# Optimization experiments

Hardware: AMD Instinct MI355X
Metric: run time of the kernel (lower is better)

The kernel has to match this reference:

```python
import math
import jax, jax.numpy as jnp
import numpy as np

SCALES = (128.0, 256.0, 512.0)
ASPECT_RATIOS = (0.5, 1.0, 2.0)
NMS_THR = 0.7
PRENMS_K = 6000   # rpn_test_prenms_topk (module built with training=False)
POST_K = 300      # rpn_test_topk
MIN_SIZE = 16.0
DW_CLIP = math.log(1000.0 / 16.0)


def conv2d(x, w, b, pad):
    y = jax.lax.conv_general_dilated(
        x, w, window_strides=(1, 1), padding=[(pad, pad), (pad, pad)],
        dimension_numbers=("NCHW", "OIHW", "NCHW"))
    return y + b[None, :, None, None]


def generate_anchors(im_h, im_w, grid_h, grid_w, dtype):
    stride_h = float(im_h // grid_h)
    stride_w = float(im_w // grid_w)
    ar = jnp.asarray(ASPECT_RATIOS, dtype)
    sc = jnp.asarray(SCALES, dtype)
    h_ratios = jnp.sqrt(ar)
    w_ratios = 1.0 / h_ratios
    hs = (h_ratios[:, None] * sc[None, :]).reshape(-1)   # [A]
    ws = (w_ratios[:, None] * sc[None, :]).reshape(-1)
    base = jnp.round(jnp.stack([-ws, -hs, ws, hs], axis=1) / 2.0)  # [A,4]
    xs = jnp.arange(grid_w, dtype=dtype) * stride_w
    ys = jnp.arange(grid_h, dtype=dtype) * stride_h
    sy, sx = jnp.meshgrid(ys, xs, indexing="ij")
    sx = sx.reshape(-1); sy = sy.reshape(-1)
    shift = jnp.stack([sx, sy, sx, sy], axis=1)           # [HW,4]
    return (shift[:, None, :] + base[None, :, :]).reshape(-1, 4)  # [HW*A,4]


def decode_boxes(pred, anchors):
    # pred, anchors: [N,4] -> decoded [N,4]
    w = anchors[:, 2] - anchors[:, 0]
    h = anchors[:, 3] - anchors[:, 1]
    cx = anchors[:, 0] + 0.5 * w
    cy = anchors[:, 1] + 0.5 * h
    dx, dy = pred[:, 0], pred[:, 1]
    dw = jnp.minimum(pred[:, 2], DW_CLIP)
    dh = jnp.minimum(pred[:, 3], DW_CLIP)
    px = dx * w + cx
    py = dy * h + cy
    pw = jnp.exp(dw) * w
    ph = jnp.exp(dh) * h
    return jnp.stack([px - 0.5 * pw, py - 0.5 * ph, px + 0.5 * pw, py + 0.5 * ph], axis=1)


def nms_keep(boxes, valid, thr):
    # boxes assumed sorted by descending score; sequential greedy NMS.
    N = boxes.shape[0]
    area = (boxes[:, 2] - boxes[:, 0]) * (boxes[:, 3] - boxes[:, 1])
    idx = jnp.arange(N)

    def body(i, keep):
        b = jax.lax.dynamic_slice(boxes, (i, 0), (1, 4))[0]
        x1 = jnp.maximum(b[0], boxes[:, 0])
        y1 = jnp.maximum(b[1], boxes[:, 1])
        x2 = jnp.minimum(b[2], boxes[:, 2])
        y2 = jnp.minimum(b[3], boxes[:, 3])
        inter = jnp.clip(x2 - x1, 0.0) * jnp.clip(y2 - y1, 0.0)
        iou = inter / (area[i] + area - inter)
        suppress = (iou > thr) & (idx > i) & keep[i]
        return keep & ~suppress

    return jax.lax.fori_loop(0, N, body, valid)


def rpn_forward(image, feat, rpn_conv_w, rpn_conv_b, cls_w, cls_b, bbox_w, bbox_b):
    rpn_feat = jax.nn.relu(conv2d(feat, rpn_conv_w, rpn_conv_b, pad=1))
    cls_scores = conv2d(rpn_feat, cls_w, cls_b, pad=0)       # [B,A,H,W]
    box_pred = conv2d(rpn_feat, bbox_w, bbox_b, pad=0)       # [B,4A,H,W]
    B, A, H, W = cls_scores.shape
    im_h, im_w = image.shape[-2], image.shape[-1]
    anchors = generate_anchors(im_h, im_w, H, W, feat.dtype)  # [HWA,4]

    cls_flat = jnp.transpose(cls_scores, (0, 2, 3, 1)).reshape(-1)              # [B*H*W*A]
    pred = jnp.transpose(box_pred.reshape(B, A, 4, H, W), (0, 3, 4, 1, 2)).reshape(-1, 4)
    proposals = decode_boxes(pred, anchors)                   # [N,4]

    scores = jax.nn.sigmoid(cls_flat)
    top_scores, top_idx = jax.lax.top_k(scores, PRENMS_K)
    props = proposals[top_idx]                                # [K,4]
    # clamp to image boundary
    props = jnp.stack([
        jnp.clip(props[:, 0], 0.0, float(im_w)),
        jnp.clip(props[:, 1], 0.0, float(im_h)),
        jnp.clip(props[:, 2], 0.0, float(im_w)),
        jnp.clip(props[:, 3], 0.0, float(im_h))], axis=1)
    w = props[:, 2] - props[:, 0]
    h = props[:, 3] - props[:, 1]
    valid = (w >= MIN_SIZE) & (h >= MIN_SIZE)
    keep = nms_keep(props, valid, NMS_THR)                    # already score-sorted
    masked = jnp.where(keep, top_scores, -jnp.inf)
    final_scores, sel = jax.lax.top_k(masked, POST_K)
    final_boxes = props[sel]
    ok = jnp.isfinite(final_scores)
    final_boxes = jnp.where(ok[:, None], final_boxes, 0.0)
    final_scores = jnp.where(ok, final_scores, 0.0)
    return jnp.concatenate([final_boxes, final_scores[:, None]], axis=1)  # [POST_K,5]


def setup_inputs() -> dict:
    key = jax.random.key(0)
    ks = jax.random.split(key, 6)
    C, H, W, A = 256, 128, 128, 9
    IMH = IMW = 1024
    std = 0.01
    return {
        "image": jax.random.normal(ks[0], (1, 3, IMH, IMW), jnp.float32),
        "feat": jax.random.normal(ks[1], (1, C, H, W), jnp.float32),
        "rpn_conv_w": jax.random.normal(ks[2], (C, C, 3, 3), jnp.float32) * std,
        "rpn_conv_b": jnp.zeros((C,), jnp.float32),
        "cls_w": jax.random.normal(ks[3], (A, C, 1, 1), jnp.float32) * std,
        "cls_b": jnp.zeros((A,), jnp.float32),
        "bbox_w": jax.random.normal(ks[4], (4 * A, C, 1, 1), jnp.float32) * std,
        "bbox_b": jnp.zeros((4 * A,), jnp.float32),
    }


def reference(image, feat, rpn_conv_w, rpn_conv_b, cls_w, cls_b, bbox_w, bbox_b):
    return rpn_forward(image, feat, rpn_conv_w, rpn_conv_b, cls_w, cls_b, bbox_w, bbox_b)
```

## Files before the change

kernel.cpp:

```cpp
#include <hip/hip_runtime.h>

#define HW 128
#define NPIX 16384
#define CIN 256
#define NSC 147456
#define PRENMS 6000
#define POSTK 300
#define DW_CLIP_F 4.135166556742356f
#define MW 96
typedef unsigned long long ull;

__global__ void wt_kernel(const float* __restrict__ w, float* __restrict__ wt,
                          unsigned* __restrict__ zp, ull* __restrict__ vb) {
    int i = blockIdx.x * 256 + threadIdx.x;
    if (i < 2304 * 256) {
        int k = i >> 8, co = i & 255;
        wt[i] = w[co * 2304 + k];
    }
    if (i < 16384 + 65536 + 64) zp[i] = 0u;
    if (i < 94) vb[i] = 0ull;
}

__global__ __launch_bounds__(256) void conv3x3_half_kernel(
    const float* __restrict__ feat, const float* __restrict__ wt,
    float* __restrict__ part)
{
    __shared__ float in_s[16 * 340];
    const int tx = threadIdx.x;
    const int ty = threadIdx.y;
    const int x0 = blockIdx.x * 32;
    const int y0 = blockIdx.y * 8;
    const int h  = blockIdx.z >> 3;
    const int co0 = (blockIdx.z & 7) << 5;
    const int tid = ty * 32 + tx;

    const int yy1 = tid / 34, xx1 = tid - yy1 * 34;
    const int t2 = tid + 256;
    const int yy2 = t2 / 34, xx2 = t2 - yy2 * 34;
    const int gy1 = y0 + yy1 - 1, gx1 = x0 + xx1 - 1;
    const int gy2 = y0 + yy2 - 1, gx2 = x0 + xx2 - 1;
    const bool p1 = ((unsigned)gy1 < 128u) && ((unsigned)gx1 < 128u);
    const bool p2 = (tid < 84) && ((unsigned)gy2 < 128u) && ((unsigned)gx2 < 128u);
    const int a1 = p1 ? (gy1 * 128 + gx1) : 0;
    const int a2 = p2 ? (gy2 * 128 + gx2) : 0;

    float acc[32];
#pragma unroll
    for (int i = 0; i < 32; ++i) acc[i] = 0.f;

    const float* fh = feat + h * 128 * NPIX;
    const float* wh = wt + h * 128 * 9 * 256;

    for (int s = 0; s < 8; ++s) {
        __syncthreads();
        const float* fbase = fh + s * 16 * NPIX;
#pragma unroll
        for (int ci = 0; ci < 16; ++ci) {
            float t = fbase[ci * NPIX + a1];
            in_s[ci * 340 + tid] = p1 ? t : 0.f;
        }
        if (tid < 84) {
#pragma unroll
            for (int ci = 0; ci < 16; ++ci) {
                float t = fbase[ci * NPIX + a2];
                in_s[ci * 340 + 256 + tid] = p2 ? t : 0.f;
            }
        }
        __syncthreads();
        const float* ws0 = wh + s * 16 * 9 * 256 + co0;
#pragma unroll 2
        for (int ci = 0; ci < 16; ++ci) {
            const float* wrow = ws0 + ci * 9 * 256;
#pragma unroll
            for (int t = 0; t < 9; ++t) {
                const int ky = t / 3, kx = t - ky * 3;
                float v = in_s[ci * 340 + (ty + ky) * 34 + (tx + kx)];
                const float* wp = wrow + t * 256;
#pragma unroll
                for (int co = 0; co < 32; ++co)
                    acc[co] = fmaf(v, wp[co], acc[co]);
            }
        }
    }
    float* po = part + h * (CIN * NPIX) + co0 * NPIX + (y0 + ty) * 128 + (x0 + tx);
#pragma unroll
    for (int co = 0; co < 32; ++co)
        po[co * NPIX] = acc[co];
}

__global__ __launch_bounds__(256) void heads_kernel(
    const float* __restrict__ part, const float* __restrict__ conv_b,
    const float* __restrict__ cls_w, const float* __restrict__ cls_b,
    const float* __restrict__ bbox_w, const float* __restrict__ bbox_b,
    float* __restrict__ scores, float* __restrict__ bb)
{
    __shared__ float wl[256][48];
    const int tid = threadIdx.x;
    for (int e = tid; e < 256 * 48; e += 256) {
        int ci = e / 48, s = e - ci * 48;
        wl[ci][s] = (s < 9) ? cls_w[s * CIN + ci]
                  : (s < 45) ? bbox_w[(s - 9) * CIN + ci] : 0.f;
    }
    __syncthreads();

    const int lane = tid & 63;
    const int sg   = tid >> 6;
    const int p    = blockIdx.x * 64 + lane;
    const int s0   = sg * 12;
    const int ns   = (sg == 3) ? 9 : 12;

    float acc[12];
#pragma unroll
    for (int i = 0; i < 12; ++i) acc[i] = 0.f;

    const float* part1 = part + CIN * NPIX;
#pragma unroll 4
    for (int ci = 0; ci < CIN; ++ci) {
        float a = part[ci * NPIX + p];
        float c = part1[ci * NPIX + p];
        float v = fmaxf(a + c + conv_b[ci], 0.f);
        const float* wr = &wl[ci][s0];
#pragma unroll
        for (int j = 0; j < 12; ++j)
            acc[j] = fmaf(v, wr[j], acc[j]);
    }
    for (int j = 0; j < ns; ++j) {
        int s = s0 + j;
        if (s < 9) {
            float sc = acc[j] + cls_b[s];
            scores[p * 9 + s] = 1.0f / (1.0f + expf(-sc));
        } else {
            bb[(s - 9) * NPIX + p] = acc[j] + bbox_b[s - 9];
        }
    }
}

__global__ __launch_bounds__(1024) void hist1_kernel(const float* __restrict__ scores,
                                                     unsigned* __restrict__ hist1) {
    __shared__ unsigned h[16384];
    const int tid = threadIdx.x;
    for (int i = tid; i < 16384; i += 1024) h[i] = 0u;
    __syncthreads();
    for (int i = blockIdx.x * 1024 + tid; i < NSC; i += gridDim.x * 1024) {
        unsigned bits = __float_as_uint(scores[i]);
        atomicAdd(&h[bits >> 16], 1u);
    }
    __syncthreads();
    for (int i = tid; i < 16384; i += 1024) {
        unsigned c = h[i];
        if (c) atomicAdd(&hist1[i], c);
    }
}

__global__ __launch_bounds__(1024) void topk_finish_kernel(
    const float* __restrict__ scores, const unsigned* __restrict__ hist1,
    unsigned* __restrict__ meta, ull* __restrict__ cand)
{
    __shared__ unsigned sh[1024];
    __shared__ unsigned g2[256];
    __shared__ unsigned res[8];
    const int tid = threadIdx.x;

    {
        unsigned local[16];
        unsigned s = 0;
#pragma unroll
        for (int i = 0; i < 16; ++i) { local[i] = hist1[tid * 16 + i]; s += local[i]; }
        sh[tid] = s;
        __syncthreads();
        for (int off = 1; off < 1024; off <<= 1) {
            unsigned v = sh[tid] + ((tid + off < 1024) ? sh[tid + off] : 0u);
            __syncthreads();
            sh[tid] = v;
            __syncthreads();
        }
        unsigned run = sh[tid] - s;
#pragma unroll
        for (int i = 15; i >= 0; --i) {
            unsigned nb = run + local[i];
            if (nb >= (unsigned)PRENMS && run < (unsigned)PRENMS) {
                res[0] = (unsigned)(tid * 16 + i);
                res[1] = run;
            }
            run = nb;
        }
    }
    __syncthreads();
    const unsigned m1 = res[0];
    const unsigned need2 = (unsigned)PRENMS - res[1];
    const uint4* s4 = (const uint4*)scores;

    if (tid < 256) g2[tid] = 0u;
    __syncthreads();
    for (int i = tid; i < NSC / 4; i += 1024) {
        uint4 v = s4[i];
        if ((v.x >> 16) == m1) atomicAdd(&g2[(v.x >> 8) & 0xFF], 1u);
        if ((v.y >> 16) == m1) atomicAdd(&g2[(v.y >> 8) & 0xFF], 1u);
        if ((v.z >> 16) == m1) atomicAdd(&g2[(v.z >> 8) & 0xFF], 1u);
        if ((v.w >> 16) == m1) atomicAdd(&g2[(v.w >> 8) & 0xFF], 1u);
    }
    __syncthreads();
    {
        unsigned hg = (tid < 256) ? g2[tid] : 0u;
        __syncthreads();
        for (int off = 1; off < 256; off <<= 1) {
            unsigned v = 0;
            if (tid < 256) v = g2[tid] + ((tid + off < 256) ? g2[tid + off] : 0u);
            __syncthreads();
            if (tid < 256) g2[tid] = v;
            __syncthreads();
        }
        if (tid < 256) {
            unsigned above = g2[tid] - hg;
            if (above < need2 && above + hg >= need2) {
                res[2] = (unsigned)tid;
                res[3] = need2 - above;
            }
        }
    }
    __syncthreads();
    const unsigned gstar = res[2];
    const unsigned need3 = res[3];
    const unsigned pref = (m1 << 8) | gstar;

    if (tid < 256) g2[tid] = 0u;
    __syncthreads();
    for (int i = tid; i < NSC / 4; i += 1024) {
        uint4 v = s4[i];
        if ((v.x >> 8) == pref) atomicAdd(&g2[v.x & 0xFF], 1u);
        if ((v.y >> 8) == pref) atomicAdd(&g2[v.y & 0xFF], 1u);
        if ((v.z >> 8) == pref) atomicAdd(&g2[v.z & 0xFF], 1u);
        if ((v.w >> 8) == pref) atomicAdd(&g2[v.w & 0xFF], 1u);
    }
    __syncthreads();
    {
        unsigned hb = (tid < 256) ? g2[tid] : 0u;
        __syncthreads();
        for (int off = 1; off < 256; off <<= 1) {
            unsigned v = 0;
            if (tid < 256) v = g2[tid] + ((tid + off < 256) ? g2[tid + off] : 0u);
            __syncthreads();
            if (tid < 256) g2[tid] = v;
            __syncthreads();
        }
        if (tid < 256) {
            unsigned above = g2[tid] - hb;
            if (above < need3 && above + hb >= need3) res[4] = (unsigned)tid;
        }
    }
    __syncthreads();
    const unsigned thr = (m1 << 16) | (gstar << 8) | res[4];

    if (tid == 0) res[5] = 0u;
    __syncthreads();
    const int lane = tid & 63;
    for (int i = tid; i < NSC / 4; i += 1024) {
        uint4 v = s4[i];
        unsigned b[4] = { v.x, v.y, v.z, v.w };
#pragma unroll
        for (int k = 0; k < 4; ++k) {
            bool pred = b[k] >= thr;
            ull bal = __ballot(pred);
            unsigned cnt = (unsigned)__popcll(bal);
            unsigned base = 0;
            if (lane == 0 && cnt) base = atomicAdd(&res[5], cnt);
            base = __shfl(base, 0);
            if (pred) {
                unsigned off = (unsigned)__popcll(bal & ((1ull << lane) - 1ull));
                unsigned pos = base + off;
                int gi = i * 4 + k;
                if (pos < 8192u)
                    cand[pos] = ((ull)b[k] << 32) | (unsigned)(~gi);
            }
        }
    }
    __syncthreads();
    if (tid == 0) meta[0] = res[5];
}

__global__ __launch_bounds__(1024) void sortA_kernel(const ull* __restrict__ cand,
                                                     const unsigned* __restrict__ meta,
                                                     ull* __restrict__ sorted) {
    __shared__ ull keys[2048];
    const int tid = threadIdx.x;
    const int base = blockIdx.x * 2048;
    const int n = min((int)meta[0], 8192);
    for (int i = tid; i < 2048; i += 1024) {
        int g = base + i;
        keys[i] = (g < n) ? cand[g] : (ull)(8191 - g);
    }
    __syncthreads();
    for (int k = 2; k <= 2048; k <<= 1) {
        for (int j = k >> 1; j >= 1; j >>= 1) {
            int s = tid;
            int i = ((s & ~(j - 1)) << 1) | (s & (j - 1));
            int p = i | j;
            ull a = keys[i], c = keys[p];
            bool desc = ((i & k) == 0);
            bool sw = desc ? (a < c) : (a > c);
            if (sw) { keys[i] = c; keys[p] = a; }
            __syncthreads();
        }
    }
    for (int i = tid; i < 2048; i += 1024) sorted[base + i] = keys[i];
}

__global__ __launch_bounds__(256) void merge_decode_kernel(
    const ull* __restrict__ sorted, const float* __restrict__ bb,
    float* __restrict__ selbox, float* __restrict__ selsc,
    ull* __restrict__ validbits)
{
    const int g = blockIdx.x * 256 + threadIdx.x;
    ull x = sorted[g];
    const int c = g >> 11;
    int rank = g & 2047;
#pragma unroll
    for (int cc = 0; cc < 4; ++cc) {
        if (cc == c) continue;
        const ull* arr = sorted + cc * 2048;
        int lo = 0, hi = 2048;
        while (lo < hi) { int mid = (lo + hi) >> 1; if (arr[mid] > x) lo = mid + 1; else hi = mid; }
        rank += lo;
    }
    if (rank < PRENMS) {
        const int r = rank;
        unsigned sbits = (unsigned)(x >> 32);
        unsigned idx = ~(unsigned)(x & 0xFFFFFFFFull);
        float score = __uint_as_float(sbits);
        int p = (int)(idx / 9u);
        int a = (int)(idx - (unsigned)p * 9u);
        int y = p >> 7, xx = p & 127;
        float d0 = bb[(a * 4 + 0) * NPIX + p];
        float d1 = bb[(a * 4 + 1) * NPIX + p];
        float d2 = bb[(a * 4 + 2) * NPIX + p];
        float d3 = bb[(a * 4 + 3) * NPIX + p];
        int ar_i = a / 3, sc_i = a - ar_i * 3;
        float arv = (ar_i == 0) ? 0.5f : ((ar_i == 1) ? 1.0f : 2.0f);
        float scv = (sc_i == 0) ? 128.f : ((sc_i == 1) ? 256.f : 512.f);
        float hr = sqrtf(arv);
        float wr = 1.0f / hr;
        float hs = hr * scv;
        float wsv = wr * scv;
        float bx1 = rintf(-wsv * 0.5f), by1 = rintf(-hs * 0.5f);
        float bx2 = rintf(wsv * 0.5f),  by2 = rintf(hs * 0.5f);
        float ax1 = xx * 8.f + bx1, ay1 = y * 8.f + by1;
        float ax2 = xx * 8.f + bx2, ay2 = y * 8.f + by2;
        float wa = ax2 - ax1, ha = ay2 - ay1;
        float cx = ax1 + 0.5f * wa, cy = ay1 + 0.5f * ha;
        float dw = fminf(d2, DW_CLIP_F), dh = fminf(d3, DW_CLIP_F);
        float px = d0 * wa + cx, py = d1 * ha + cy;
        float pw = expf(dw) * wa, ph = expf(dh) * ha;
        float x1 = px - 0.5f * pw, y1 = py - 0.5f * ph;
        float x2 = px + 0.5f * pw, y2 = py + 0.5f * ph;
        x1 = fminf(fmaxf(x1, 0.f), 1024.f);
        y1 = fminf(fmaxf(y1, 0.f), 1024.f);
        x2 = fminf(fmaxf(x2, 0.f), 1024.f);
        y2 = fminf(fmaxf(y2, 0.f), 1024.f);
        float bw = x2 - x1, bh = y2 - y1;
        bool valid = (bw >= 16.f) && (bh >= 16.f);
        selbox[r * 4 + 0] = x1; selbox[r * 4 + 1] = y1;
        selbox[r * 4 + 2] = x2; selbox[r * 4 + 3] = y2;
        selsc[r] = score;
        if (valid) atomicOr(&validbits[r >> 6], 1ull << (r & 63));
    }
}

__global__ __launch_bounds__(256) void maskbuild_kernel(
    const float* __restrict__ selbox, ull* __restrict__ mask)
{
    __shared__ float jb0[64], jb1[64], jb2[64], jb3[64];
    const int jw = blockIdx.y;
    const int tid = threadIdx.x;
    const int i = blockIdx.x * 256 + tid;
    if (jw * 64 + 63 < blockIdx.x * 256) {
        if (i < PRENMS) mask[(size_t)i * MW + jw] = 0ull;
        return;
    }
    if (tid < 64) {
        int j = jw * 64 + tid;
        float x1 = 0.f, y1 = 0.f, x2 = 0.f, y2 = 0.f;
        if (j < PRENMS) {
            x1 = selbox[j * 4 + 0]; y1 = selbox[j * 4 + 1];
            x2 = selbox[j * 4 + 2]; y2 = selbox[j * 4 + 3];
        }
        jb0[tid] = x1; jb1[tid] = y1; jb2[tid] = x2; jb3[tid] = y2;
    }
    __syncthreads();
    if (i >= PRENMS) return;
    const float ix1 = selbox[i * 4 + 0], iy1 = selbox[i * 4 + 1];
    const float ix2 = selbox[i * 4 + 2], iy2 = selbox[i * 4 + 3];
    const float iarea = (ix2 - ix1) * (iy2 - iy1);
    ull word = 0ull;
    for (int b = 0; b < 64; ++b) {
        int j = jw * 64 + b;
        float xx1 = fmaxf(ix1, jb0[b]);
        float yy1 = fmaxf(iy1, jb1[b]);
        float xx2 = fminf(ix2, jb2[b]);
        float yy2 = fminf(iy2, jb3[b]);
        float iw = fmaxf(xx2 - xx1, 0.f);
        float ih = fmaxf(yy2 - yy1, 0.f);
        float inter = iw * ih;
        float jarea = (jb2[b] - jb0[b]) * (jb3[b] - jb1[b]);
        float iou = inter / (iarea + jarea - inter);
        if (j > i && iou > 0.7f) word |= (1ull << b);
    }
    mask[(size_t)i * MW + jw] = word;
}

__global__ __launch_bounds__(64) void nms_scan_kernel(
    const ull* __restrict__ validbits,
    const ull* __restrict__ mask,
    const float* __restrict__ selbox, const float* __restrict__ selsc,
    float* __restrict__ out)
{
    __shared__ int kept[POSTK];
    const int l = threadIdx.x;
    ull supp0 = ~validbits[l];
    ull supp1 = (l < 30) ? ~validbits[64 + l] : ~0ull;
    int nk = 0;
    ull ownrow_next = mask[(size_t)l * MW + 0];
    for (int wi = 0; wi < 94 && nk < POSTK; ++wi) {
        ull ownrow = ownrow_next;
        if (wi < 93) ownrow_next = mask[(size_t)((wi + 1) * 64 + l) * MW + (wi + 1)];
        ull wsup = (wi < 64) ? __shfl(supp0, wi) : __shfl(supp1, wi - 64);
        ull active = ~wsup;
        if (!active) continue;
        ull keptbits = 0ull;
        while (active && nk < POSTK) {
            int b = __builtin_ctzll(active);
            keptbits |= (1ull << b);
            if (l == 0) kept[nk] = wi * 64 + b;
            nk++;
            ull rowb = __shfl(ownrow, b);
            ull gt = (b == 63) ? 0ull : (~0ull << (b + 1));
            active &= gt & ~rowb;
        }
        while (keptbits) {
            int b0 = __builtin_ctzll(keptbits); keptbits &= keptbits - 1;
            int b1 = -1, b2 = -1, b3 = -1;
            if (keptbits) { b1 = __builtin_ctzll(keptbits); keptbits &= keptbits - 1; }
            if (keptbits) { b2 = __builtin_ctzll(keptbits); keptbits &= keptbits - 1; }
            if (keptbits) { b3 = __builtin_ctzll(keptbits); keptbits &= keptbits - 1; }
            const ull* r0 = mask + (size_t)(wi * 64 + b0) * MW;
            ull t0a = r0[l], t0b = (l < 30) ? r0[64 + l] : 0ull;
            ull t1a = 0, t1b = 0, t2a = 0, t2b = 0, t3a = 0, t3b = 0;
            if (b1 >= 0) { const ull* r1 = mask + (size_t)(wi * 64 + b1) * MW; t1a = r1[l]; t1b = (l < 30) ? r1[64 + l] : 0ull; }
            if (b2 >= 0) { const ull* r2 = mask + (size_t)(wi * 64 + b2) * MW; t2a = r2[l]; t2b = (l < 30) ? r2[64 + l] : 0ull; }
            if (b3 >= 0) { const ull* r3 = mask + (size_t)(wi * 64 + b3) * MW; t3a = r3[l]; t3b = (l < 30) ? r3[64 + l] : 0ull; }
            supp0 |= t0a | t1a | t2a | t3a;
            supp1 |= t0b | t1b | t2b | t3b;
        }
    }
    __syncthreads();
    for (int r = l; r < POSTK; r += 64) {
        if (r < nk) {
            int i = kept[r];
            out[r * 5 + 0] = selbox[i * 4 + 0];
            out[r * 5 + 1] = selbox[i * 4 + 1];
            out[r * 5 + 2] = selbox[i * 4 + 2];
            out[r * 5 + 3] = selbox[i * 4 + 3];
            out[r * 5 + 4] = selsc[i];
        } else {
            out[r * 5 + 0] = 0.f; out[r * 5 + 1] = 0.f;
            out[r * 5 + 2] = 0.f; out[r * 5 + 3] = 0.f;
            out[r * 5 + 4] = 0.f;
        }
    }
}

extern "C" void kernel_launch(void* const* d_in, const int* in_sizes, int n_in,
                              void* d_out, int out_size, void* d_ws, size_t ws_size,
                              hipStream_t stream) {
    const float* feat    = (const float*)d_in[1];
    const float* conv_w  = (const float*)d_in[2];
    const float* conv_b  = (const float*)d_in[3];
    const float* cls_w   = (const float*)d_in[4];
    const float* cls_b   = (const float*)d_in[5];
    const float* bbox_w  = (const float*)d_in[6];
    const float* bbox_b  = (const float*)d_in[7];
    float* out = (float*)d_out;

    char* ws = (char*)d_ws;
    float*    part      = (float*)(ws + 0);
    float*    wt        = (float*)(ws + 33554432);
    float*    bb        = (float*)(ws + 35913728);
    float*    scores    = (float*)(ws + 38273024);
    unsigned* hist1     = (unsigned*)(ws + 38862848);
    unsigned* meta      = (unsigned*)(ws + 39190528);
    ull*      cand      = (ull*)(ws + 39190784);
    ull*      sorted    = (ull*)(ws + 39256320);
    float*    selbox    = (float*)(ws + 39387392);
    float*    selsc     = (float*)(ws + 39483648);
    ull*      validbits = (ull*)(ws + 39507712);
    ull*      mask      = (ull*)(ws + 39508480);

    wt_kernel<<<2304, 256, 0, stream>>>(conv_w, wt, hist1, validbits);
    conv3x3_half_kernel<<<dim3(4, 16, 16), dim3(32, 8), 0, stream>>>(feat, wt, part);
    heads_kernel<<<256, 256, 0, stream>>>(part, conv_b, cls_w, cls_b, bbox_w, bbox_b, scores, bb);
    hist1_kernel<<<64, 1024, 0, stream>>>(scores, hist1);
    topk_finish_kernel<<<1, 1024, 0, stream>>>(scores, hist1, meta, cand);
    sortA_kernel<<<4, 1024, 0, stream>>>(cand, meta, sorted);
    merge_decode_kernel<<<32, 256, 0, stream>>>(sorted, bb, selbox, selsc, validbits);
    maskbuild_kernel<<<dim3(24, 94), 256, 0, stream>>>(selbox, mask);
    nms_scan_kernel<<<1, 64, 0, stream>>>(validbits, mask, selbox, selsc, out);
}
```

Measured before the change: 519.2 us.

## Fuse bitonic sort and merge-decode into a single-block 8192-key sort kernel

Replaces the four-block 2048-key bitonic sort plus the binary-search merge/decode kernel with one 1024-thread block that bitonic-sorts all 8192 candidates in 64KB of shared memory and decodes the top 6000 directly. This removes one kernel launch, the global round trip of the sorted array, and the per-element binary searches. In exchange the sort runs on a single CU with more bitonic stages (91 barriers, each thread handling four compare-swaps per stage) instead of being spread over four blocks.

```diff
diff --git a/kernel.cpp b/kernel.cpp
--- a/kernel.cpp
+++ b/kernel.cpp
@@ -278,52 +278,33 @@
     if (tid == 0) meta[0] = res[5];
 }
 
-__global__ __launch_bounds__(1024) void sortA_kernel(const ull* __restrict__ cand,
-                                                     const unsigned* __restrict__ meta,
-                                                     ull* __restrict__ sorted) {
-    __shared__ ull keys[2048];
-    const int tid = threadIdx.x;
-    const int base = blockIdx.x * 2048;
-    const int n = min((int)meta[0], 8192);
-    for (int i = tid; i < 2048; i += 1024) {
-        int g = base + i;
-        keys[i] = (g < n) ? cand[g] : (ull)(8191 - g);
-    }
-    __syncthreads();
-    for (int k = 2; k <= 2048; k <<= 1) {
-        for (int j = k >> 1; j >= 1; j >>= 1) {
-            int s = tid;
-            int i = ((s & ~(j - 1)) << 1) | (s & (j - 1));
-            int p = i | j;
-            ull a = keys[i], c = keys[p];
-            bool desc = ((i & k) == 0);
-            bool sw = desc ? (a < c) : (a > c);
-            if (sw) { keys[i] = c; keys[p] = a; }
-            __syncthreads();
-        }
-    }
-    for (int i = tid; i < 2048; i += 1024) sorted[base + i] = keys[i];
-}
-
-__global__ __launch_bounds__(256) void merge_decode_kernel(
-    const ull* __restrict__ sorted, const float* __restrict__ bb,
+__global__ __launch_bounds__(1024) void sort_decode_kernel(
+    const ull* __restrict__ cand, const unsigned* __restrict__ meta,
+    const float* __restrict__ bb,
     float* __restrict__ selbox, float* __restrict__ selsc,
     ull* __restrict__ validbits)
 {
-    const int g = blockIdx.x * 256 + threadIdx.x;
-    ull x = sorted[g];
-    const int c = g >> 11;
-    int rank = g & 2047;
-#pragma unroll
-    for (int cc = 0; cc < 4; ++cc) {
-        if (cc == c) continue;
-        const ull* arr = sorted + cc * 2048;
-        int lo = 0, hi = 2048;
-        while (lo < hi) { int mid = (lo + hi) >> 1; if (arr[mid] > x) lo = mid + 1; else hi = mid; }
-        rank += lo;
-    }
-    if (rank < PRENMS) {
-        const int r = rank;
+    __shared__ ull keys[8192];
+    const int tid = threadIdx.x;
+    const int n = min((int)meta[0], 8192);
+    for (int i = tid; i < 8192; i += 1024)
+        keys[i] = (i < n) ? cand[i] : (ull)(8191 - i);
+    __syncthreads();
+    for (int k = 2; k <= 8192; k <<= 1) {
+        for (int j = k >> 1; j >= 1; j >>= 1) {
+            for (int s = tid; s < 4096; s += 1024) {
+                int i = ((s & ~(j - 1)) << 1) | (s & (j - 1));
+                int p = i | j;
+                ull a = keys[i], c = keys[p];
+                bool desc = ((i & k) == 0);
+                bool sw = desc ? (a < c) : (a > c);
+                if (sw) { keys[i] = c; keys[p] = a; }
+            }
+            __syncthreads();
+        }
+    }
+    for (int r = tid; r < PRENMS; r += 1024) {
+        ull x = keys[r];
         unsigned sbits = (unsigned)(x >> 32);
         unsigned idx = ~(unsigned)(x & 0xFFFFFFFFull);
         float score = __uint_as_float(sbits);
@@ -488,7 +469,6 @@
     unsigned* hist1     = (unsigned*)(ws + 38862848);
     unsigned* meta      = (unsigned*)(ws + 39190528);
     ull*      cand      = (ull*)(ws + 39190784);
-    ull*      sorted    = (ull*)(ws + 39256320);
     float*    selbox    = (float*)(ws + 39387392);
     float*    selsc     = (float*)(ws + 39483648);
     ull*      validbits = (ull*)(ws + 39507712);
@@ -499,8 +479,7 @@
     heads_kernel<<<256, 256, 0, stream>>>(part, conv_b, cls_w, cls_b, bbox_w, bbox_b, scores, bb);
     hist1_kernel<<<64, 1024, 0, stream>>>(scores, hist1);
     topk_finish_kernel<<<1, 1024, 0, stream>>>(scores, hist1, meta, cand);
-    sortA_kernel<<<4, 1024, 0, stream>>>(cand, meta, sorted);
-    merge_decode_kernel<<<32, 256, 0, stream>>>(sorted, bb, selbox, selsc, validbits);
+    sort_decode_kernel<<<1, 1024, 0, stream>>>(cand, meta, bb, selbox, selsc, validbits);
     maskbuild_kernel<<<dim3(24, 94), 256, 0, stream>>>(selbox, mask);
     nms_scan_kernel<<<1, 64, 0, stream>>>(validbits, mask, selbox, selsc, out);
 }
```

Result: slower. 659.6 us (+27.0%).
